# Performance work log

Measured on AMD Instinct MI355X. Metric: run time of the kernel, lower is better.

Reference implementation:

```python
import jax, jax.numpy as jnp
import numpy as np

B, TL, TG, K, H = 32, 4096, 1, 128, 8


def setup_inputs() -> dict:
    key = jax.random.key(0)
    ks = jax.random.split(key, 7)
    return {
        "x_local": jax.random.normal(ks[0], (B, TL, K), jnp.float32),
        "x_glob": jax.random.normal(ks[1], (B, TG, K), jnp.float32),
        # weights stored (in_features, out_features) so y = x @ W, matching torch Linear math
        "Wq": jax.random.normal(ks[2], (K, K * H), jnp.float32) / np.sqrt(K).astype(np.float32),
        "Wk": jax.random.normal(ks[3], (K, K * H), jnp.float32) / np.sqrt(K).astype(np.float32),
        "Wv": jax.random.normal(ks[4], (K, K * H), jnp.float32) / np.sqrt(K).astype(np.float32),
        "Wu": jax.random.normal(ks[5], (H * K, K), jnp.float32) / np.sqrt(H * K).astype(np.float32),
        "bu": jnp.zeros((K,), jnp.float32),
    }


def reference(x_local, x_glob, Wq, Wk, Wv, Wu, bu):
    b, t_l, k = x_local.shape
    t_g = x_glob.shape[1]
    h = Wq.shape[1] // k
    scale = k ** -0.25  # applied to both q and k, as in the original

    # projections -> (b, h, t, k)
    q = (x_glob @ Wq).reshape(b, t_g, h, k).transpose(0, 2, 1, 3) * scale
    kk = (x_local @ Wk).reshape(b, t_l, h, k).transpose(0, 2, 1, 3) * scale
    v = (x_local @ Wv).reshape(b, t_l, h, k).transpose(0, 2, 1, 3)

    # dot = bmm(q, k^T).transpose(1,2) -> (b, h, t_l, t_g)
    dot = jnp.einsum('bhgk,bhlk->bhlg', q, kk)
    # softmax over t_l (dim=1 of the (bh, t_l, t_g) tensor in torch)
    attn = jax.nn.softmax(dot, axis=2)  # dropout rate 0 -> identity

    # elementwise mul (t_g==1 broadcasts against k) then sum over t_l
    out = attn * v                                  # (b, h, t_l, k)
    out = out.transpose(0, 2, 1, 3).reshape(b, t_l, h * k)
    out = out.sum(axis=1)                           # (b, h*k)
    return out @ Wu + bu                            # (b, k)
```

## Files before the change

### kernel.cpp

```cpp
#include <hip/hip_runtime.h>

#define BB 32
#define TL 4096
#define KK 128
#define HH 8
#define SCALE2 0.08838834764831845f

#define NCH 8

#define OFF_WK  0
#define N_WK    (BB*HH*KK)
#define OFF_XA  (OFF_WK + N_WK)
#define N_XA    (BB*NCH*HH*KK)
#define OFF_DEN (OFF_XA + N_XA)
#define N_DEN   (BB*NCH*HH)

__global__ __launch_bounds__(128) void sa_kA(
    const float* __restrict__ xg, const float* __restrict__ Wq,
    const float* __restrict__ Wk, float* __restrict__ wk_eff) {
  int bh = blockIdx.x;
  int b = bh >> 3, h = bh & 7;
  int t = threadIdx.x;
  __shared__ float xgs[KK];
  __shared__ float qh[KK];
  xgs[t] = xg[b * KK + t];
  __syncthreads();
  float acc = 0.f;
  const float* wq = Wq + h * KK + t;
  for (int c2 = 0; c2 < KK; ++c2) acc += xgs[c2] * wq[c2 * (HH * KK)];
  qh[t] = acc;
  __syncthreads();
  const float4* wk4 = (const float4*)(Wk + t * (HH * KK) + h * KK);
  const float4* qh4 = (const float4*)qh;
  float acc2 = 0.f;
  #pragma unroll 8
  for (int c4 = 0; c4 < KK / 4; ++c4) {
    float4 a = wk4[c4];
    float4 q4 = qh4[c4];
    acc2 += a.x * q4.x + a.y * q4.y + a.z * q4.z + a.w * q4.w;
  }
  wk_eff[bh * KK + t] = acc2 * SCALE2;
}

__global__ __launch_bounds__(512) void sa_kF(
    const float* __restrict__ x, const float* __restrict__ wk_eff,
    float* __restrict__ xattnP, float* __restrict__ denP) {
  const int chunk = blockIdx.x;
  const int b = blockIdx.y;
  const int t = threadIdx.x;
  const int lane16 = t & 15;
  const int g = t >> 4;

  float wkr[HH][8];
  const float* wkb = wk_eff + (b * HH) * KK + lane16 * 8;
  #pragma unroll
  for (int h = 0; h < HH; ++h) {
    float4 a = *(const float4*)(wkb + h * KK);
    float4 c = *(const float4*)(wkb + h * KK + 4);
    wkr[h][0] = a.x; wkr[h][1] = a.y; wkr[h][2] = a.z; wkr[h][3] = a.w;
    wkr[h][4] = c.x; wkr[h][5] = c.y; wkr[h][6] = c.z; wkr[h][7] = c.w;
  }
  float acc[HH][8];
  float den[HH];
  #pragma unroll
  for (int h = 0; h < HH; ++h) {
    den[h] = 0.f;
    #pragma unroll
    for (int j = 0; j < 8; ++j) acc[h][j] = 0.f;
  }

  const int rows = TL / NCH;
  const int l0 = chunk * rows;
  #pragma unroll 2
  for (int i = 0; i < rows / 32; ++i) {
    const int l = l0 + i * 32 + g;
    const float* xr = x + ((size_t)(b * TL + l)) * KK + lane16 * 8;
    float4 xa = *(const float4*)xr;
    float4 xb = *(const float4*)(xr + 4);
    float part[HH];
    #pragma unroll
    for (int h = 0; h < HH; ++h) {
      part[h] = xa.x * wkr[h][0] + xa.y * wkr[h][1] + xa.z * wkr[h][2] + xa.w * wkr[h][3]
              + xb.x * wkr[h][4] + xb.y * wkr[h][5] + xb.z * wkr[h][6] + xb.w * wkr[h][7];
    }
    #pragma unroll
    for (int s = 1; s < 16; s <<= 1) {
      #pragma unroll
      for (int h = 0; h < HH; ++h) part[h] += __shfl_xor(part[h], s, 64);
    }
    #pragma unroll
    for (int h = 0; h < HH; ++h) {
      float p = __expf(part[h]);
      den[h] += p;
      acc[h][0] += p * xa.x; acc[h][1] += p * xa.y;
      acc[h][2] += p * xa.z; acc[h][3] += p * xa.w;
      acc[h][4] += p * xb.x; acc[h][5] += p * xb.y;
      acc[h][6] += p * xb.z; acc[h][7] += p * xb.w;
    }
  }

  #pragma unroll
  for (int h = 0; h < HH; ++h) {
    #pragma unroll
    for (int j = 0; j < 8; ++j) {
      acc[h][j] += __shfl_xor(acc[h][j], 16, 64);
      acc[h][j] += __shfl_xor(acc[h][j], 32, 64);
    }
    den[h] += __shfl_xor(den[h], 16, 64);
    den[h] += __shfl_xor(den[h], 32, 64);
  }

  __shared__ float red[8][HH * KK];
  __shared__ float redD[8][HH];
  const int wv = t >> 6, ln = t & 63;
  if (ln < 16) {
    #pragma unroll
    for (int h = 0; h < HH; ++h)
      #pragma unroll
      for (int j = 0; j < 8; ++j)
        red[wv][h * KK + ln * 8 + j] = acc[h][j];
    if (ln < HH) redD[wv][ln] = den[ln];
  }
  __syncthreads();
  const size_t base = ((size_t)(b * NCH + chunk)) * (HH * KK);
  for (int e = t; e < HH * KK; e += 512) {
    float s = 0.f;
    #pragma unroll
    for (int w = 0; w < 8; ++w) s += red[w][e];
    xattnP[base + e] = s;
  }
  if (t < HH) {
    float s = 0.f;
    #pragma unroll
    for (int w = 0; w < 8; ++w) s += redD[w][t];
    denP[(b * NCH + chunk) * HH + t] = s;
  }
}

__global__ __launch_bounds__(512) void sa_kE(
    const float* __restrict__ xattnP, const float* __restrict__ denP,
    const float* __restrict__ Wv, const float* __restrict__ Wu,
    const float* __restrict__ bu, float* __restrict__ out) {
  const int b = blockIdx.x;
  const int t = threadIdx.x;
  __shared__ float uS[HH][KK + 1];
  __shared__ float sS[HH * KK];
  __shared__ float dS[HH];
  __shared__ float oS[4][KK];

  if (t < HH) {
    float d = 0.f;
    #pragma unroll
    for (int ch = 0; ch < NCH; ++ch) d += denP[(b * NCH + ch) * HH + t];
    dS[t] = d;
  }
  __syncthreads();
  for (int e = t; e < HH * KK; e += 512) {
    float a = 0.f;
    #pragma unroll
    for (int ch = 0; ch < NCH; ++ch)
      a += xattnP[((size_t)(b * NCH + ch)) * (HH * KK) + e];
    uS[e >> 7][e & 127] = a / dS[e >> 7];
  }
  __syncthreads();
  for (int e = t; e < HH * KK; e += 512) {
    const int h = e >> 7;
    const float* wv = Wv + e;
    const float* uh = uS[h];
    float sv = 0.f;
    #pragma unroll 8
    for (int c = 0; c < KK; ++c) sv += uh[c] * wv[(size_t)c * (HH * KK)];
    sS[e] = sv;
  }
  __syncthreads();
  const int cp = t & 127, q = t >> 7;
  float po = 0.f;
  const float* wu = Wu + cp;
  #pragma unroll 8
  for (int k = q * 256; k < (q + 1) * 256; ++k) po += sS[k] * wu[(size_t)k * KK];
  oS[q][cp] = po;
  __syncthreads();
  if (t < KK) out[b * KK + t] = oS[0][t] + oS[1][t] + oS[2][t] + oS[3][t] + bu[t];
}

extern "C" void kernel_launch(void* const* d_in, const int* in_sizes, int n_in,
                              void* d_out, int out_size, void* d_ws, size_t ws_size,
                              hipStream_t stream) {
  const float* x  = (const float*)d_in[0];
  const float* xg = (const float*)d_in[1];
  const float* Wq = (const float*)d_in[2];
  const float* Wk = (const float*)d_in[3];
  const float* Wv = (const float*)d_in[4];
  const float* Wu = (const float*)d_in[5];
  const float* bu = (const float*)d_in[6];
  float* out = (float*)d_out;

  float* ws     = (float*)d_ws;
  float* wk_eff = ws + OFF_WK;
  float* xattnP = ws + OFF_XA;
  float* denP   = ws + OFF_DEN;

  sa_kA<<<dim3(BB * HH), dim3(128), 0, stream>>>(xg, Wq, Wk, wk_eff);
  sa_kF<<<dim3(NCH, BB), dim3(512), 0, stream>>>(x, wk_eff, xattnP, denP);
  sa_kE<<<dim3(BB), dim3(512), 0, stream>>>(xattnP, denP, Wv, Wu, bu, out);
}
```

Before: 61.52 us.

## Use DPP transpose-reduce for head dots and split L into more chunks

The main streaming kernel now reduces the eight per-head partial dots with a butterfly transpose-reduce built from DPP and ds_swizzle. Each lane ends up holding one head's dot, so only one exp per lane is computed instead of eight, and the exp results are redistributed the same way. It also splits the sequence into 32 chunks with 256-thread blocks and prefetches the next row, giving more blocks and better latency hiding. The epilogue kernel uses 1024 threads with one element per thread. The cost is more partial results to combine and more complex lane-permutation logic.

```diff
diff --git a/kernel.cpp b/kernel.cpp
--- a/kernel.cpp
+++ b/kernel.cpp
@@ -6,7 +6,7 @@
 #define HH 8
 #define SCALE2 0.08838834764831845f
 
-#define NCH 8
+#define NCH 32
 
 #define OFF_WK  0
 #define N_WK    (BB*HH*KK)
@@ -14,6 +14,19 @@
 #define N_XA    (BB*NCH*HH*KK)
 #define OFF_DEN (OFF_XA + N_XA)
 #define N_DEN   (BB*NCH*HH)
+
+__device__ __forceinline__ float dpp_xor1(float v) {
+  return __int_as_float(__builtin_amdgcn_update_dpp(0, __float_as_int(v), 0xB1, 0xF, 0xF, true));
+}
+__device__ __forceinline__ float dpp_xor2(float v) {
+  return __int_as_float(__builtin_amdgcn_update_dpp(0, __float_as_int(v), 0x4E, 0xF, 0xF, true));
+}
+__device__ __forceinline__ float dpp_xor8(float v) {
+  return __int_as_float(__builtin_amdgcn_update_dpp(0, __float_as_int(v), 0x128, 0xF, 0xF, true));
+}
+__device__ __forceinline__ float swz_xor4(float v) {
+  return __int_as_float(__builtin_amdgcn_ds_swizzle(__float_as_int(v), 0x101F));
+}
 
 __global__ __launch_bounds__(128) void sa_kA(
     const float* __restrict__ xg, const float* __restrict__ Wq,
@@ -27,6 +40,7 @@
   __syncthreads();
   float acc = 0.f;
   const float* wq = Wq + h * KK + t;
+  #pragma unroll 8
   for (int c2 = 0; c2 < KK; ++c2) acc += xgs[c2] * wq[c2 * (HH * KK)];
   qh[t] = acc;
   __syncthreads();
@@ -42,111 +56,128 @@
   wk_eff[bh * KK + t] = acc2 * SCALE2;
 }
 
-__global__ __launch_bounds__(512) void sa_kF(
+__global__ __launch_bounds__(256, 3) void sa_kF(
     const float* __restrict__ x, const float* __restrict__ wk_eff,
     float* __restrict__ xattnP, float* __restrict__ denP) {
   const int chunk = blockIdx.x;
   const int b = blockIdx.y;
   const int t = threadIdx.x;
   const int lane16 = t & 15;
-  const int g = t >> 4;
+  const int g16 = t >> 4;
 
   float wkr[HH][8];
-  const float* wkb = wk_eff + (b * HH) * KK + lane16 * 8;
+  {
+    const float* wkb = wk_eff + (b * HH) * KK + lane16 * 8;
+    #pragma unroll
+    for (int h = 0; h < HH; ++h) {
+      float4 a = *(const float4*)(wkb + h * KK);
+      float4 c = *(const float4*)(wkb + h * KK + 4);
+      wkr[h][0] = a.x; wkr[h][1] = a.y; wkr[h][2] = a.z; wkr[h][3] = a.w;
+      wkr[h][4] = c.x; wkr[h][5] = c.y; wkr[h][6] = c.z; wkr[h][7] = c.w;
+    }
+  }
+  float acc[HH][8];
   #pragma unroll
-  for (int h = 0; h < HH; ++h) {
-    float4 a = *(const float4*)(wkb + h * KK);
-    float4 c = *(const float4*)(wkb + h * KK + 4);
-    wkr[h][0] = a.x; wkr[h][1] = a.y; wkr[h][2] = a.z; wkr[h][3] = a.w;
-    wkr[h][4] = c.x; wkr[h][5] = c.y; wkr[h][6] = c.z; wkr[h][7] = c.w;
-  }
-  float acc[HH][8];
-  float den[HH];
-  #pragma unroll
-  for (int h = 0; h < HH; ++h) {
-    den[h] = 0.f;
-    #pragma unroll
-    for (int j = 0; j < 8; ++j) acc[h][j] = 0.f;
-  }
+  for (int s = 0; s < HH; ++s)
+    #pragma unroll
+    for (int j = 0; j < 8; ++j) acc[s][j] = 0.f;
+  float den1 = 0.f;
 
   const int rows = TL / NCH;
   const int l0 = chunk * rows;
-  #pragma unroll 2
-  for (int i = 0; i < rows / 32; ++i) {
-    const int l = l0 + i * 32 + g;
-    const float* xr = x + ((size_t)(b * TL + l)) * KK + lane16 * 8;
-    float4 xa = *(const float4*)xr;
-    float4 xb = *(const float4*)(xr + 4);
+  const float* xr = x + ((size_t)(b * TL + l0 + g16)) * KK + lane16 * 8;
+  float4 xa = *(const float4*)xr;
+  float4 xb = *(const float4*)(xr + 4);
+  const bool hi8 = (t & 8) != 0, hi4 = (t & 4) != 0, hi2 = (t & 2) != 0;
+
+  for (int i = 0; i < rows / 16; ++i) {
+    float4 na = xa, nb = xb;
+    if (i + 1 < rows / 16) {
+      const float* xn = xr + 16 * KK;
+      na = *(const float4*)xn; nb = *(const float4*)(xn + 4);
+    }
     float part[HH];
     #pragma unroll
-    for (int h = 0; h < HH; ++h) {
+    for (int h = 0; h < HH; ++h)
       part[h] = xa.x * wkr[h][0] + xa.y * wkr[h][1] + xa.z * wkr[h][2] + xa.w * wkr[h][3]
               + xb.x * wkr[h][4] + xb.y * wkr[h][5] + xb.z * wkr[h][6] + xb.w * wkr[h][7];
-    }
-    #pragma unroll
-    for (int s = 1; s < 16; s <<= 1) {
-      #pragma unroll
-      for (int h = 0; h < HH; ++h) part[h] += __shfl_xor(part[h], s, 64);
-    }
-    #pragma unroll
-    for (int h = 0; h < HH; ++h) {
-      float p = __expf(part[h]);
-      den[h] += p;
-      acc[h][0] += p * xa.x; acc[h][1] += p * xa.y;
-      acc[h][2] += p * xa.z; acc[h][3] += p * xa.w;
-      acc[h][4] += p * xb.x; acc[h][5] += p * xb.y;
-      acc[h][6] += p * xb.z; acc[h][7] += p * xb.w;
-    }
+    float r8[4];
+    #pragma unroll
+    for (int s = 0; s < 4; ++s) {
+      float mine = hi8 ? part[s + 4] : part[s];
+      float oth  = hi8 ? part[s]     : part[s + 4];
+      r8[s] = mine + dpp_xor8(oth);
+    }
+    float r4[2];
+    #pragma unroll
+    for (int s = 0; s < 2; ++s) {
+      float mine = hi4 ? r8[s + 2] : r8[s];
+      float oth  = hi4 ? r8[s]     : r8[s + 2];
+      r4[s] = mine + swz_xor4(oth);
+    }
+    float m2 = hi2 ? r4[1] : r4[0];
+    float o2 = hi2 ? r4[0] : r4[1];
+    float r2 = m2 + dpp_xor2(o2);
+    float dotv = r2 + dpp_xor1(r2);
+    float p0 = __expf(dotv);
+    den1 += p0;
+    float p_[8];
+    p_[0] = p0;
+    p_[1] = dpp_xor2(p0);
+    p_[2] = swz_xor4(p0);   p_[3] = swz_xor4(p_[1]);
+    p_[4] = dpp_xor8(p0);   p_[5] = dpp_xor8(p_[1]);
+    p_[6] = dpp_xor8(p_[2]); p_[7] = dpp_xor8(p_[3]);
+    #pragma unroll
+    for (int s = 0; s < HH; ++s) {
+      acc[s][0] += p_[s] * xa.x; acc[s][1] += p_[s] * xa.y;
+      acc[s][2] += p_[s] * xa.z; acc[s][3] += p_[s] * xa.w;
+      acc[s][4] += p_[s] * xb.x; acc[s][5] += p_[s] * xb.y;
+      acc[s][6] += p_[s] * xb.z; acc[s][7] += p_[s] * xb.w;
+    }
+    xa = na; xb = nb; xr += 16 * KK;
   }
 
   #pragma unroll
-  for (int h = 0; h < HH; ++h) {
+  for (int s = 0; s < HH; ++s)
     #pragma unroll
     for (int j = 0; j < 8; ++j) {
-      acc[h][j] += __shfl_xor(acc[h][j], 16, 64);
-      acc[h][j] += __shfl_xor(acc[h][j], 32, 64);
-    }
-    den[h] += __shfl_xor(den[h], 16, 64);
-    den[h] += __shfl_xor(den[h], 32, 64);
-  }
-
-  __shared__ float red[8][HH * KK];
-  __shared__ float redD[8][HH];
+      acc[s][j] += __shfl_xor(acc[s][j], 16, 64);
+      acc[s][j] += __shfl_xor(acc[s][j], 32, 64);
+    }
+  den1 += __shfl_xor(den1, 16, 64);
+  den1 += __shfl_xor(den1, 32, 64);
+
+  __shared__ float red[4][HH * KK];
+  __shared__ float redD[4][HH];
   const int wv = t >> 6, ln = t & 63;
   if (ln < 16) {
-    #pragma unroll
-    for (int h = 0; h < HH; ++h)
+    const int g = (ln >> 1) & 7;
+    #pragma unroll
+    for (int s = 0; s < HH; ++s) {
+      const int h = g ^ s;
       #pragma unroll
-      for (int j = 0; j < 8; ++j)
-        red[wv][h * KK + ln * 8 + j] = acc[h][j];
-    if (ln < HH) redD[wv][ln] = den[ln];
+      for (int j = 0; j < 8; ++j) red[wv][h * KK + ln * 8 + j] = acc[s][j];
+    }
+    if ((ln & 1) == 0) redD[wv][g] = den1;
   }
   __syncthreads();
   const size_t base = ((size_t)(b * NCH + chunk)) * (HH * KK);
-  for (int e = t; e < HH * KK; e += 512) {
-    float s = 0.f;
-    #pragma unroll
-    for (int w = 0; w < 8; ++w) s += red[w][e];
-    xattnP[base + e] = s;
-  }
-  if (t < HH) {
-    float s = 0.f;
-    #pragma unroll
-    for (int w = 0; w < 8; ++w) s += redD[w][t];
-    denP[(b * NCH + chunk) * HH + t] = s;
-  }
-}
-
-__global__ __launch_bounds__(512) void sa_kE(
+  for (int e = t; e < HH * KK; e += 256)
+    xattnP[base + e] = red[0][e] + red[1][e] + red[2][e] + red[3][e];
+  if (t < HH)
+    denP[(b * NCH + chunk) * HH + t] = redD[0][t] + redD[1][t] + redD[2][t] + redD[3][t];
+}
+
+__global__ __launch_bounds__(1024) void sa_kE(
     const float* __restrict__ xattnP, const float* __restrict__ denP,
     const float* __restrict__ Wv, const float* __restrict__ Wu,
     const float* __restrict__ bu, float* __restrict__ out) {
   const int b = blockIdx.x;
   const int t = threadIdx.x;
-  __shared__ float uS[HH][KK + 1];
+  __shared__ float uS[HH * KK];
   __shared__ float sS[HH * KK];
   __shared__ float dS[HH];
-  __shared__ float oS[4][KK];
+  __shared__ float oS[8][KK];
 
   if (t < HH) {
     float d = 0.f;
@@ -155,32 +186,37 @@
     dS[t] = d;
   }
   __syncthreads();
-  for (int e = t; e < HH * KK; e += 512) {
+  {
     float a = 0.f;
-    #pragma unroll
+    #pragma unroll 8
     for (int ch = 0; ch < NCH; ++ch)
-      a += xattnP[((size_t)(b * NCH + ch)) * (HH * KK) + e];
-    uS[e >> 7][e & 127] = a / dS[e >> 7];
-  }
-  __syncthreads();
-  for (int e = t; e < HH * KK; e += 512) {
-    const int h = e >> 7;
-    const float* wv = Wv + e;
-    const float* uh = uS[h];
+      a += xattnP[((size_t)(b * NCH + ch)) * (HH * KK) + t];
+    uS[t] = a / dS[t >> 7];
+  }
+  __syncthreads();
+  {
+    const float* uh = uS + (t >> 7) * KK;
     float sv = 0.f;
     #pragma unroll 8
-    for (int c = 0; c < KK; ++c) sv += uh[c] * wv[(size_t)c * (HH * KK)];
-    sS[e] = sv;
-  }
-  __syncthreads();
-  const int cp = t & 127, q = t >> 7;
-  float po = 0.f;
-  const float* wu = Wu + cp;
-  #pragma unroll 8
-  for (int k = q * 256; k < (q + 1) * 256; ++k) po += sS[k] * wu[(size_t)k * KK];
-  oS[q][cp] = po;
-  __syncthreads();
-  if (t < KK) out[b * KK + t] = oS[0][t] + oS[1][t] + oS[2][t] + oS[3][t] + bu[t];
+    for (int c = 0; c < KK; ++c) sv += uh[c] * Wv[(size_t)c * (HH * KK) + t];
+    sS[t] = sv;
+  }
+  __syncthreads();
+  {
+    const int cp = t & 127, q = t >> 7;
+    float po = 0.f;
+    #pragma unroll 8
+    for (int k = q * KK; k < (q + 1) * KK; ++k)
+      po += sS[k] * Wu[(size_t)k * KK + cp];
+    oS[q][cp] = po;
+  }
+  __syncthreads();
+  if (t < KK) {
+    float o = bu[t];
+    #pragma unroll
+    for (int q = 0; q < 8; ++q) o += oS[q][t];
+    out[b * KK + t] = o;
+  }
 }
 
 extern "C" void kernel_launch(void* const* d_in, const int* in_sizes, int n_in,
@@ -201,6 +237,6 @@
   float* denP   = ws + OFF_DEN;
 
   sa_kA<<<dim3(BB * HH), dim3(128), 0, stream>>>(xg, Wq, Wk, wk_eff);
-  sa_kF<<<dim3(NCH, BB), dim3(512), 0, stream>>>(x, wk_eff, xattnP, denP);
-  sa_kE<<<dim3(BB), dim3(512), 0, stream>>>(xattnP, denP, Wv, Wu, bu, out);
-}
+  sa_kF<<<dim3(NCH, BB), dim3(256), 0, stream>>>(x, wk_eff, xattnP, denP);
+  sa_kE<<<dim3(BB), dim3(1024), 0, stream>>>(xattnP, denP, Wv, Wu, bu, out);
+}
```

Measured after the change: 51.47 us. 1.2x faster.
